# Kernel optimization log

Hardware: AMD Instinct MI355X
Metric: run time of the kernel (lower is better)

Reference implementation:

```python
import jax, jax.numpy as jnp
import numpy as np
import math

D_MODEL = 1024
NUM_HEADS = 16
D_K = D_MODEL // NUM_HEADS
THETA = 10000.0
BATCH = 2
SEQ = 2048


def setup_inputs() -> dict:
    key = jax.random.key(0)
    k = jax.random.split(key, 6)
    scale = 1.0 / math.sqrt(D_MODEL)
    in_features = jax.random.normal(k[0], (BATCH, SEQ, D_MODEL), dtype=jnp.float32)
    token_positions = jnp.sort(
        jax.random.randint(k[1], (BATCH, SEQ), 0, SEQ), axis=-1
    ).astype(jnp.int32)
    q_proj_weight = jax.random.normal(k[2], (D_MODEL, D_MODEL), dtype=jnp.float32) * scale
    k_proj_weight = jax.random.normal(k[3], (D_MODEL, D_MODEL), dtype=jnp.float32) * scale
    v_proj_weight = jax.random.normal(k[4], (D_MODEL, D_MODEL), dtype=jnp.float32) * scale
    o_proj_weight = jax.random.normal(k[5], (D_MODEL, D_MODEL), dtype=jnp.float32) * scale
    return {
        "in_features": in_features,
        "token_positions": token_positions,
        "q_proj_weight": q_proj_weight,
        "k_proj_weight": k_proj_weight,
        "v_proj_weight": v_proj_weight,
        "o_proj_weight": o_proj_weight,
    }


def _apply_rope(x, positions):
    # x: [b, h, s, d_k]; positions: [b, s]
    freqs = 1.0 / (THETA ** (jnp.arange(0, D_K, 2, dtype=jnp.float32) / D_K))  # [d_k/2]
    angles = positions[:, None, :, None].astype(jnp.float32) * freqs  # [b,1,s,d_k/2]
    cos, sin = jnp.cos(angles), jnp.sin(angles)
    x1 = x[..., 0::2]
    x2 = x[..., 1::2]
    x1r = x1 * cos - x2 * sin
    x2r = x1 * sin + x2 * cos
    # interleave pairs back: stack on new last axis then flatten
    return jnp.stack([x1r, x2r], axis=-1).reshape(x.shape)


def reference(in_features, token_positions, q_proj_weight, k_proj_weight,
              v_proj_weight, o_proj_weight):
    b, s, _ = in_features.shape
    Q = jnp.einsum('bsi,di->bsd', in_features, q_proj_weight)
    K = jnp.einsum('bsi,di->bsd', in_features, k_proj_weight)
    V = jnp.einsum('bsi,di->bsd', in_features, v_proj_weight)
    # split heads: [b, h, s, d_k]
    def split(x):
        return x.reshape(b, s, NUM_HEADS, D_K).transpose(0, 2, 1, 3)
    Q, K, V = split(Q), split(K), split(V)
    Q = _apply_rope(Q, token_positions)
    K = _apply_rope(K, token_positions)
    scores = jnp.einsum('bhqd,bhkd->bhqk', Q, K) / math.sqrt(D_K)
    causal = jnp.tril(jnp.ones((s, s), dtype=bool))  # allowed positions
    scores = jnp.where(causal[None, None], scores, -jnp.inf)
    weights = jax.nn.softmax(scores, axis=-1)
    head_out = jnp.einsum('bhqk,bhkd->bhqd', weights, V)
    combined = head_out.transpose(0, 2, 1, 3).reshape(b, s, D_MODEL)
    return jnp.einsum('bsd,od->bso', combined, o_proj_weight)
```

## Files before the change

kernel.cpp:

```cpp
#include <hip/hip_runtime.h>
#include <hip/hip_bf16.h>
#include <stdint.h>

#define DMODEL 1024
#define NH 16
#define DKH 64
#define BB 2
#define SS 2048
#define MTOT (BB*SS)

#define BK 32
#define TP 136

using f32x4  = __attribute__((ext_vector_type(4))) float;
using bf16x8 = __attribute__((ext_vector_type(8))) __bf16;

#define GLL(g, l) __builtin_amdgcn_global_load_lds( \
    (const __attribute__((address_space(1))) unsigned int*)(g), \
    (__attribute__((address_space(3))) unsigned int*)(l), 16, 0, 0)

__device__ __forceinline__ unsigned short f2bf(float f) {
  union { float f; uint32_t u; } v; v.f = f;
  uint32_t r = v.u + 0x7FFFu + ((v.u >> 16) & 1u);
  return (unsigned short)(r >> 16);
}

__global__ __launch_bounds__(256) void cvt_all(
    const float* __restrict__ X,
    const float* __restrict__ w0, const float* __restrict__ w1,
    const float* __restrict__ w2, const float* __restrict__ w3,
    unsigned short* __restrict__ Xb,
    unsigned short* __restrict__ Wb)
{
  const int bid = blockIdx.x;
  const float* src;
  unsigned short* dst;
  int i;
  if (bid < 2048) {
    src = X; dst = Xb; i = bid * 256 + threadIdx.x;
  } else {
    int t = bid - 2048;
    int z = t >> 9;
    src = (z == 0) ? w0 : (z == 1) ? w1 : (z == 2) ? w2 : w3;
    dst = Wb + (size_t)z * DMODEL * DMODEL;
    i = (t & 511) * 256 + threadIdx.x;
  }
  const float4* s4 = (const float4*)src;
  float4 a = s4[2*i], b = s4[2*i+1];
  uint4 o;
  o.x = (uint32_t)f2bf(a.x) | ((uint32_t)f2bf(a.y) << 16);
  o.y = (uint32_t)f2bf(a.z) | ((uint32_t)f2bf(a.w) << 16);
  o.z = (uint32_t)f2bf(b.x) | ((uint32_t)f2bf(b.y) << 16);
  o.w = (uint32_t)f2bf(b.z) | ((uint32_t)f2bf(b.w) << 16);
  *(uint4*)(dst + (size_t)i * 8) = o;
}

template<int MI, int NI>
__device__ __forceinline__ void gemm_pipe(
    const unsigned short* __restrict__ A,
    const unsigned short* __restrict__ Bw,
    int m0, int n0, int K,
    unsigned short* As, unsigned short* Bs,
    f32x4 (&acc)[MI][NI])
{
  const int BMl = MI * 32;
  const int BNl = NI * 32;
  const int tid = threadIdx.x;
  const int lane = tid & 63;
  const int w = tid >> 6;
  const int wr = w >> 1, wc = w & 1;
  const int lrow = lane & 15;
  const int g = lane >> 4;

  const f32x4 fzero = {0.f, 0.f, 0.f, 0.f};
  #pragma unroll
  for (int i = 0; i < MI; ++i)
    #pragma unroll
    for (int j = 0; j < NI; ++j)
      acc[i][j] = fzero;

  const int nk = K / BK;

  auto STAGE = [&](int k0, int buf) {
    #pragma unroll
    for (int c = 0; c < MI / 2; ++c) {
      int i = tid + c * 256;
      int row = i >> 2, cc = i & 3;
      int sc = cc ^ ((row >> 1) & 3);
      GLL(A + (size_t)(m0 + row) * K + k0 + sc * 8, As + buf * (BMl * BK) + i * 8);
    }
    #pragma unroll
    for (int c = 0; c < NI / 2; ++c) {
      int i = tid + c * 256;
      int row = i >> 2, cc = i & 3;
      int sc = cc ^ ((row >> 1) & 3);
      GLL(Bw + (size_t)(n0 + row) * K + k0 + sc * 8, Bs + buf * (BNl * BK) + i * 8);
    }
  };

  STAGE(0, 0);
  __syncthreads();
  for (int t = 0; t < nk; ++t) {
    const int cur = t & 1;
    if (t + 1 < nk) STAGE((t + 1) * BK, cur ^ 1);

    const unsigned short* Ab = As + cur * (BMl * BK);
    const unsigned short* Bb = Bs + cur * (BNl * BK);
    bf16x8 af[MI], bfr[NI];
    #pragma unroll
    for (int mi = 0; mi < MI; ++mi) {
      int row = wr * (MI * 16) + mi * 16 + lrow;
      af[mi] = *(const bf16x8*)(Ab + row * BK + (g ^ ((row >> 1) & 3)) * 8);
    }
    #pragma unroll
    for (int ni = 0; ni < NI; ++ni) {
      int row = wc * (NI * 16) + ni * 16 + lrow;
      bfr[ni] = *(const bf16x8*)(Bb + row * BK + (g ^ ((row >> 1) & 3)) * 8);
    }
    #pragma unroll
    for (int mi = 0; mi < MI; ++mi)
      #pragma unroll
      for (int ni = 0; ni < NI; ++ni)
        acc[mi][ni] = __builtin_amdgcn_mfma_f32_16x16x32_bf16(af[mi], bfr[ni], acc[mi][ni], 0, 0, 0);

    __syncthreads();
  }
}

__global__ __launch_bounds__(256) void gemm_qkv(
    const unsigned short* __restrict__ Xb,
    const unsigned short* __restrict__ Wf,
    const int* __restrict__ tpos,
    unsigned short* __restrict__ Qh,
    unsigned short* __restrict__ Kh,
    unsigned short* __restrict__ Vt)
{
  __shared__ __align__(16) unsigned char smraw[128 * TP * 2];
  unsigned short* sm = (unsigned short*)smraw;
  unsigned short* As = sm;
  unsigned short* Bs = sm + 2 * 128 * BK;

  const int m0 = blockIdx.x * 128;
  const int n0 = blockIdx.y * 128;
  const int z  = n0 >> 10;
  const int nloc = n0 & 1023;

  f32x4 acc[4][4];
  gemm_pipe<4, 4>(Xb, Wf, m0, n0, DMODEL, As, Bs, acc);

  const int tid  = threadIdx.x;
  const int lane = tid & 63;
  const int w    = tid >> 6;
  const int wr   = w >> 1, wc = w & 1;
  const int cb   = lane & 15, rb = (lane >> 4) * 4;

  if (z < 2) {
    #pragma unroll
    for (int mi = 0; mi < 4; ++mi)
      #pragma unroll
      for (int ni = 0; ni < 4; ++ni)
        #pragma unroll
        for (int r = 0; r < 4; ++r)
          sm[(wr * 64 + mi * 16 + rb + r) * TP + wc * 64 + ni * 16 + cb] = f2bf(acc[mi][ni][r]);
  } else {
    #pragma unroll
    for (int mi = 0; mi < 4; ++mi)
      #pragma unroll
      for (int ni = 0; ni < 4; ++ni)
        #pragma unroll
        for (int r = 0; r < 4; ++r)
          sm[(wc * 64 + ni * 16 + cb) * TP + wr * 64 + mi * 16 + rb + r] = f2bf(acc[mi][ni][r]);
  }
  __syncthreads();

  const int b = m0 >> 11;
  const float l2t = 13.28771237954945f / 32.0f;
  const float qsc = (z == 0) ? 0.18033688011112042f : 1.0f;

  if (z < 2) {
    unsigned short* dst = (z == 0) ? Qh : Kh;
    #pragma unroll
    for (int p = 0; p < 8; ++p) {
      const int m_l = p * 16 + (tid >> 4);
      const int ck  = tid & 15;
      bf16x8 vals = *(const bf16x8*)(sm + m_l * TP + ck * 8);
      const int m = m0 + m_l, s = m & (SS - 1);
      const int pos = tpos[m];
      const int n = nloc + ck * 8, h = n >> 6, dh = n & 63;
      union { unsigned short u[8]; uint4 v; } ov;
      #pragma unroll
      for (int e = 0; e < 4; ++e) {
        float x1 = (float)vals[2 * e], x2 = (float)vals[2 * e + 1];
        int j = (dh >> 1) + e;
        float ang = (float)pos * exp2f(-(float)j * l2t);
        float sn, cs;
        __sincosf(ang, &sn, &cs);
        sn *= qsc; cs *= qsc;
        ov.u[2 * e]     = f2bf(x1 * cs - x2 * sn);
        ov.u[2 * e + 1] = f2bf(x1 * sn + x2 * cs);
      }
      *(uint4*)(dst + ((size_t)(b * NH + h) * SS + s) * DKH + dh) = ov.v;
    }
  } else {
    #pragma unroll
    for (int p = 0; p < 8; ++p) {
      const int n_l = p * 16 + (tid >> 4);
      const int ck  = tid & 15;
      bf16x8 vals = *(const bf16x8*)(sm + n_l * TP + ck * 8);
      const int n = nloc + n_l, h = n >> 6, dh = n & 63;
      const int m = m0 + ck * 8, s = m & (SS - 1);
      *(bf16x8*)(Vt + ((size_t)(b * NH + h) * DKH + dh) * SS + s) = vals;
    }
  }
}

__global__ __launch_bounds__(256) void attn(
    const unsigned short* __restrict__ Qh,
    const unsigned short* __restrict__ Kh,
    const unsigned short* __restrict__ Vt,
    unsigned short* __restrict__ comb)
{
  __shared__ unsigned short Ks[2][64 * 64];
  __shared__ unsigned short Vs[2][64 * 64];
  __shared__ unsigned short Ps[4][32 * 64];

  const int idx = blockIdx.x;
  const int x = idx & 7;
  const int o = idx >> 3;
  const int bh = x * 4 + (o & 3);
  const int j = o >> 2;
  const int qt = (j < 8) ? j : 23 - j;

  const int tid = threadIdx.x, lane = tid & 63, w = tid >> 6;
  const int lc = lane & 15, lh = lane >> 4;

  const unsigned short* kb = Kh + (size_t)bh * SS * DKH;
  const unsigned short* vb = Vt + (size_t)bh * DKH * SS;
  const int b = bh >> 4, h = bh & 15;
  const f32x4 fzero = {0.f, 0.f, 0.f, 0.f};
  const int Q0 = qt * 128;

  auto STAGE = [&](int t, int buf) {
    const int kv0 = t * 64;
    #pragma unroll
    for (int c = 0; c < 2; ++c) {
      int i = tid + c * 256;
      int row = i >> 3, pc = i & 7;
      int sc = pc ^ (row & 7);
      GLL(kb + (size_t)(kv0 + row) * DKH + sc * 8, &Ks[buf][i * 8]);
      GLL(vb + (size_t)row * SS + kv0 + sc * 8, &Vs[buf][i * 8]);
    }
  };

  bf16x8 qf[2][2];
  #pragma unroll
  for (int qg = 0; qg < 2; ++qg) {
    const unsigned short* Qb = Qh + ((size_t)bh * SS + Q0 + w * 32 + qg * 16 + lc) * DKH;
    qf[qg][0] = *(const bf16x8*)(Qb + lh * 8);
    qf[qg][1] = *(const bf16x8*)(Qb + lh * 8 + 32);
  }

  f32x4 oacc[2][4];
  #pragma unroll
  for (int qg = 0; qg < 2; ++qg)
    #pragma unroll
    for (int i = 0; i < 4; ++i) oacc[qg][i] = fzero;
  float lsum[2] = {0.f, 0.f};
  unsigned short* psw = &Ps[w][0];

  auto QK = [&](int cur, f32x4 (&sacc)[2][4]) {
    __builtin_amdgcn_s_setprio(1);
    #pragma unroll
    for (int nf = 0; nf < 4; ++nf) {
      const int row = nf * 16 + lc;
      bf16x8 kf0 = *(const bf16x8*)(&Ks[cur][row * 64 + ((lh) ^ (row & 7)) * 8]);
      bf16x8 kf1 = *(const bf16x8*)(&Ks[cur][row * 64 + ((lh + 4) ^ (row & 7)) * 8]);
      #pragma unroll
      for (int qg = 0; qg < 2; ++qg) {
        sacc[qg][nf] = __builtin_amdgcn_mfma_f32_16x16x32_bf16(kf0, qf[qg][0], fzero, 0, 0, 0);
        sacc[qg][nf] = __builtin_amdgcn_mfma_f32_16x16x32_bf16(kf1, qf[qg][1], sacc[qg][nf], 0, 0, 0);
      }
    }
    __builtin_amdgcn_s_setprio(0);
  };

  auto SM = [&](f32x4 (&sacc)[2][4], bool domask, int t) {
    #pragma unroll
    for (int qg = 0; qg < 2; ++qg) {
      float sv[4][4];
      if (domask) {
        const int kv0 = t * 64;
        const int qlane = Q0 + w * 32 + qg * 16 + lc;
        #pragma unroll
        for (int nf = 0; nf < 4; ++nf)
          #pragma unroll
          for (int r = 0; r < 4; ++r) {
            float x2 = sacc[qg][nf][r];
            if ((kv0 + nf * 16 + lh * 4 + r) > qlane) x2 = -1e30f;
            sv[nf][r] = x2;
          }
      } else {
        #pragma unroll
        for (int nf = 0; nf < 4; ++nf)
          #pragma unroll
          for (int r = 0; r < 4; ++r)
            sv[nf][r] = sacc[qg][nf][r];
      }
      float rs = 0.f;
      #pragma unroll
      for (int nf = 0; nf < 4; ++nf)
        #pragma unroll
        for (int r = 0; r < 4; ++r) {
          float p = exp2f(sv[nf][r]);
          sv[nf][r] = p;
          rs += p;
        }
      lsum[qg] += rs;
      #pragma unroll
      for (int nf = 0; nf < 4; ++nf) {
        uint32_t u0, u1;
        asm("v_cvt_pk_bf16_f32 %0, %1, %2" : "=v"(u0) : "v"(sv[nf][0]), "v"(sv[nf][1]));
        asm("v_cvt_pk_bf16_f32 %0, %1, %2" : "=v"(u1) : "v"(sv[nf][2]), "v"(sv[nf][3]));
        int swz = (nf * 2 + (lh >> 1)) ^ (lc & 7);
        uint32_t* p = (uint32_t*)&psw[(qg * 16 + lc) * 64 + swz * 8 + (lh & 1) * 4];
        p[0] = u0; p[1] = u1;
      }
    }
  };

  auto PV = [&](int cur) {
    __builtin_amdgcn_s_setprio(1);
    #pragma unroll
    for (int c = 0; c < 2; ++c) {
      bf16x8 pf[2];
      #pragma unroll
      for (int qg = 0; qg < 2; ++qg)
        pf[qg] = *(const bf16x8*)(&psw[(qg * 16 + lc) * 64 + ((c * 4 + lh) ^ (lc & 7)) * 8]);
      #pragma unroll
      for (int df = 0; df < 4; ++df) {
        const int row = df * 16 + lc;
        bf16x8 vf = *(const bf16x8*)(&Vs[cur][row * 64 + ((c * 4 + lh) ^ (row & 7)) * 8]);
        #pragma unroll
        for (int qg = 0; qg < 2; ++qg)
          oacc[qg][df] = __builtin_amdgcn_mfma_f32_16x16x32_bf16(pf[qg], vf, oacc[qg][df], 0, 0, 0);
      }
    }
    __builtin_amdgcn_s_setprio(0);
  };

  const int nt = 2 * qt + 2;
  STAGE(0, 0);
  for (int t = 0; t < 2 * qt; ++t) {
    const int cur = t & 1;
    asm volatile("s_waitcnt vmcnt(0)" ::: "memory");
    __builtin_amdgcn_s_barrier();
    f32x4 sacc[2][4];
    QK(cur, sacc);
    STAGE(t + 1, cur ^ 1);
    SM(sacc, false, t);
    PV(cur);
  }
  #pragma unroll
  for (int tt = 0; tt < 2; ++tt) {
    const int t = 2 * qt + tt;
    const int cur = t & 1;
    asm volatile("s_waitcnt vmcnt(0)" ::: "memory");
    __builtin_amdgcn_s_barrier();
    f32x4 sacc[2][4];
    QK(cur, sacc);
    if (t + 1 < nt) STAGE(t + 1, cur ^ 1);
    SM(sacc, true, t);
    PV(cur);
  }

  #pragma unroll
  for (int qg = 0; qg < 2; ++qg) {
    float ls0 = lsum[qg];
    ls0 += __shfl_xor(ls0, 16);
    ls0 += __shfl_xor(ls0, 32);
    #pragma unroll
    for (int r = 0; r < 4; ++r) {
      float ls = __shfl(ls0, lh * 4 + r);
      float inv = 1.f / ls;
      const int q = Q0 + w * 32 + qg * 16 + lh * 4 + r;
      #pragma unroll
      for (int df = 0; df < 4; ++df) {
        const int d = h * 64 + df * 16 + lc;
        comb[((size_t)(b * SS + q)) * DMODEL + d] = f2bf(oacc[qg][df][r] * inv);
      }
    }
  }
}

__global__ __launch_bounds__(256) void gemm_out(
    const unsigned short* __restrict__ Cb,
    const unsigned short* __restrict__ Wob,
    float* __restrict__ out)
{
  __shared__ __align__(16) unsigned char smraw[128 * TP * 2];
  unsigned short* As = (unsigned short*)smraw;
  unsigned short* Bs = (unsigned short*)smraw + 2 * 128 * BK;
  float* smf = (float*)smraw;

  const int m0 = blockIdx.x * 128, n0 = blockIdx.y * 64;
  f32x4 acc[4][2];
  gemm_pipe<4, 2>(Cb, Wob, m0, n0, DMODEL, As, Bs, acc);

  const int tid  = threadIdx.x;
  const int lane = tid & 63;
  const int w    = tid >> 6;
  const int wr   = w >> 1, wc = w & 1;
  const int cb   = lane & 15, rb = (lane >> 4) * 4;

  #pragma unroll
  for (int mi = 0; mi < 4; ++mi)
    #pragma unroll
    for (int ni = 0; ni < 2; ++ni)
      #pragma unroll
      for (int r = 0; r < 4; ++r)
        smf[(wr * 64 + mi * 16 + rb + r) * 68 + wc * 32 + ni * 16 + cb] = acc[mi][ni][r];
  __syncthreads();

  #pragma unroll
  for (int p = 0; p < 8; ++p) {
    const int row = p * 16 + (tid >> 4);
    const int ck  = tid & 15;
    float4 vv = *(const float4*)(smf + row * 68 + ck * 4);
    *(float4*)(out + (size_t)(m0 + row) * DMODEL + n0 + ck * 4) = vv;
  }
}

extern "C" void kernel_launch(void* const* d_in, const int* in_sizes, int n_in,
                              void* d_out, int out_size, void* d_ws, size_t ws_size,
                              hipStream_t stream) {
  (void)in_sizes; (void)n_in; (void)out_size; (void)ws_size;
  const float* X    = (const float*)d_in[0];
  const int*   tpos = (const int*)d_in[1];
  const float* Wq   = (const float*)d_in[2];
  const float* Wk   = (const float*)d_in[3];
  const float* Wv   = (const float*)d_in[4];
  const float* Wo   = (const float*)d_in[5];
  float* out = (float*)d_out;

  uint8_t* ws = (uint8_t*)d_ws;
  const size_t SZ_X = (size_t)MTOT * DMODEL * 2;
  const size_t SZ_W = (size_t)DMODEL * DMODEL * 2;
  const size_t SZ_H = (size_t)BB * NH * SS * DKH * 2;
  unsigned short* Xb   = (unsigned short*)(ws);
  unsigned short* Wqb  = (unsigned short*)(ws + SZ_X);
  unsigned short* Wob  = (unsigned short*)(ws + SZ_X + 3 * SZ_W);
  unsigned short* Qh   = (unsigned short*)(ws + SZ_X + 4 * SZ_W);
  unsigned short* Kh   = (unsigned short*)(ws + SZ_X + 4 * SZ_W + SZ_H);
  unsigned short* Vt   = (unsigned short*)(ws + SZ_X + 4 * SZ_W + 2 * SZ_H);
  unsigned short* comb = Xb;

  cvt_all<<<dim3(4096), dim3(256), 0, stream>>>(X, Wq, Wk, Wv, Wo, Xb, Wqb);

  gemm_qkv<<<dim3(MTOT / 128, 24), dim3(256), 0, stream>>>(Xb, Wqb, tpos, Qh, Kh, Vt);
  attn<<<dim3(512), dim3(256), 0, stream>>>(Qh, Kh, Vt, comb);
  gemm_out<<<dim3(MTOT / 128, 16), dim3(256), 0, stream>>>(comb, Wob, out);
}
```

Measured before the change: 112.7 us.

## Enlarge attention KV tiles to 128 and remap GEMM blocks for XCD locality

The attention kernel now stages 128-row K/V tiles per barrier and processes them as two 64-wide halves, which halves the number of barriers and wait points per query tile. LDS use per block doubles, which may reduce occupancy. Both GEMMs also remap block indices so that each XCD handles a contiguous range of N tiles, aiming for better L2 reuse of weight columns.

```diff
diff --git a/kernel.cpp b/kernel.cpp
--- a/kernel.cpp
+++ b/kernel.cpp
@@ -140,8 +140,10 @@
   unsigned short* As = sm;
   unsigned short* Bs = sm + 2 * 128 * BK;
 
-  const int m0 = blockIdx.x * 128;
-  const int n0 = blockIdx.y * 128;
+  const int bid = blockIdx.x + 32 * blockIdx.y;
+  const int xcd = bid & 7, oo = bid >> 3;
+  const int m0 = (oo & 31) * 128;
+  const int n0 = (xcd * 3 + (oo >> 5)) * 128;
   const int z  = n0 >> 10;
   const int nloc = n0 & 1023;
 
@@ -220,8 +222,8 @@
     const unsigned short* __restrict__ Vt,
     unsigned short* __restrict__ comb)
 {
-  __shared__ unsigned short Ks[2][64 * 64];
-  __shared__ unsigned short Vs[2][64 * 64];
+  __shared__ unsigned short Ks[2][128 * 64];
+  __shared__ unsigned short Vs[2][64 * 128];
   __shared__ unsigned short Ps[4][32 * 64];
 
   const int idx = blockIdx.x;
@@ -241,13 +243,19 @@
   const int Q0 = qt * 128;
 
   auto STAGE = [&](int t, int buf) {
-    const int kv0 = t * 64;
-    #pragma unroll
-    for (int c = 0; c < 2; ++c) {
+    const int kv0 = t * 128;
+    #pragma unroll
+    for (int c = 0; c < 4; ++c) {
       int i = tid + c * 256;
       int row = i >> 3, pc = i & 7;
       int sc = pc ^ (row & 7);
       GLL(kb + (size_t)(kv0 + row) * DKH + sc * 8, &Ks[buf][i * 8]);
+    }
+    #pragma unroll
+    for (int c = 0; c < 4; ++c) {
+      int i = tid + c * 256;
+      int row = i >> 4, cc = i & 15;
+      int sc = cc ^ (row & 7);
       GLL(vb + (size_t)row * SS + kv0 + sc * 8, &Vs[buf][i * 8]);
     }
   };
@@ -268,11 +276,11 @@
   float lsum[2] = {0.f, 0.f};
   unsigned short* psw = &Ps[w][0];
 
-  auto QK = [&](int cur, f32x4 (&sacc)[2][4]) {
+  auto QK = [&](int cur, int hh, f32x4 (&sacc)[2][4]) {
     __builtin_amdgcn_s_setprio(1);
     #pragma unroll
     for (int nf = 0; nf < 4; ++nf) {
-      const int row = nf * 16 + lc;
+      const int row = hh * 64 + nf * 16 + lc;
       bf16x8 kf0 = *(const bf16x8*)(&Ks[cur][row * 64 + ((lh) ^ (row & 7)) * 8]);
       bf16x8 kf1 = *(const bf16x8*)(&Ks[cur][row * 64 + ((lh + 4) ^ (row & 7)) * 8]);
       #pragma unroll
@@ -284,12 +292,12 @@
     __builtin_amdgcn_s_setprio(0);
   };
 
-  auto SM = [&](f32x4 (&sacc)[2][4], bool domask, int t) {
+  auto SM = [&](f32x4 (&sacc)[2][4], bool domask, int t, int hh) {
     #pragma unroll
     for (int qg = 0; qg < 2; ++qg) {
       float sv[4][4];
       if (domask) {
-        const int kv0 = t * 64;
+        const int kv0 = t * 128 + hh * 64;
         const int qlane = Q0 + w * 32 + qg * 16 + lc;
         #pragma unroll
         for (int nf = 0; nf < 4; ++nf)
@@ -328,7 +336,7 @@
     }
   };
 
-  auto PV = [&](int cur) {
+  auto PV = [&](int cur, int hh) {
     __builtin_amdgcn_s_setprio(1);
     #pragma unroll
     for (int c = 0; c < 2; ++c) {
@@ -339,7 +347,7 @@
       #pragma unroll
       for (int df = 0; df < 4; ++df) {
         const int row = df * 16 + lc;
-        bf16x8 vf = *(const bf16x8*)(&Vs[cur][row * 64 + ((c * 4 + lh) ^ (row & 7)) * 8]);
+        bf16x8 vf = *(const bf16x8*)(&Vs[cur][row * 128 + ((hh * 8 + c * 4 + lh) ^ (row & 7)) * 8]);
         #pragma unroll
         for (int qg = 0; qg < 2; ++qg)
           oacc[qg][df] = __builtin_amdgcn_mfma_f32_16x16x32_bf16(pf[qg], vf, oacc[qg][df], 0, 0, 0);
@@ -348,29 +356,31 @@
     __builtin_amdgcn_s_setprio(0);
   };
 
-  const int nt = 2 * qt + 2;
   STAGE(0, 0);
-  for (int t = 0; t < 2 * qt; ++t) {
+  for (int t = 0; t < qt; ++t) {
     const int cur = t & 1;
     asm volatile("s_waitcnt vmcnt(0)" ::: "memory");
     __builtin_amdgcn_s_barrier();
     f32x4 sacc[2][4];
-    QK(cur, sacc);
+    QK(cur, 0, sacc);
     STAGE(t + 1, cur ^ 1);
-    SM(sacc, false, t);
-    PV(cur);
-  }
-  #pragma unroll
-  for (int tt = 0; tt < 2; ++tt) {
-    const int t = 2 * qt + tt;
-    const int cur = t & 1;
+    SM(sacc, false, t, 0);
+    PV(cur, 0);
+    QK(cur, 1, sacc);
+    SM(sacc, false, t, 1);
+    PV(cur, 1);
+  }
+  {
+    const int cur = qt & 1;
     asm volatile("s_waitcnt vmcnt(0)" ::: "memory");
     __builtin_amdgcn_s_barrier();
     f32x4 sacc[2][4];
-    QK(cur, sacc);
-    if (t + 1 < nt) STAGE(t + 1, cur ^ 1);
-    SM(sacc, true, t);
-    PV(cur);
+    QK(cur, 0, sacc);
+    SM(sacc, true, qt, 0);
+    PV(cur, 0);
+    QK(cur, 1, sacc);
+    SM(sacc, true, qt, 1);
+    PV(cur, 1);
   }
 
   #pragma unroll
@@ -402,7 +412,11 @@
   unsigned short* Bs = (unsigned short*)smraw + 2 * 128 * BK;
   float* smf = (float*)smraw;
 
-  const int m0 = blockIdx.x * 128, n0 = blockIdx.y * 64;
+  const int bid = blockIdx.x + 32 * blockIdx.y;
+  const int xcd = bid & 7, oo = bid >> 3;
+  const int m0 = (oo & 31) * 128;
+  const int n0 = (xcd * 2 + (oo >> 5)) * 64;
+
   f32x4 acc[4][2];
   gemm_pipe<4, 2>(Cb, Wob, m0, n0, DMODEL, As, Bs, acc);
 
@@ -456,7 +470,7 @@
 
   cvt_all<<<dim3(4096), dim3(256), 0, stream>>>(X, Wq, Wk, Wv, Wo, Xb, Wqb);
 
-  gemm_qkv<<<dim3(MTOT / 128, 24), dim3(256), 0, stream>>>(Xb, Wqb, tpos, Qh, Kh, Vt);
+  gemm_qkv<<<dim3(32, 24), dim3(256), 0, stream>>>(Xb, Wqb, tpos, Qh, Kh, Vt);
   attn<<<dim3(512), dim3(256), 0, stream>>>(Qh, Kh, Vt, comb);
-  gemm_out<<<dim3(MTOT / 128, 16), dim3(256), 0, stream>>>(comb, Wob, out);
-}
+  gemm_out<<<dim3(32, 16), dim3(256), 0, stream>>>(comb, Wob, out);
+}
```

After: 118.6 us. 1.05x slower.
